# Kernel tuning notes

Measured on AMD Instinct MI355X. Metric: run time of the kernel, lower is better.

## Reference

```python
import jax, jax.numpy as jnp
import numpy as np

EPS = 1e-5

def _layer_norm(y, w, b):
    mu = y.mean(-1, keepdims=True)
    var = jnp.mean((y - mu) ** 2, axis=-1, keepdims=True)
    return (y - mu) * jax.lax.rsqrt(var + EPS) * w + b


def setup_inputs() -> dict:
    key = jax.random.key(0)
    ks = jax.random.split(key, 8)
    B, D, H, W = 1, 96, 96, 96
    N, R, K = 16, 6, 4
    x = jax.random.normal(ks[0], (B, D, H, W), jnp.float32)
    x_proj_weight = jax.random.normal(ks[1], (K, R + 2 * N, D), jnp.float32) * 0.05
    dt_projs_weight = jax.random.normal(ks[2], (K, D, R), jnp.float32) * 0.1
    dt_projs_bias = jax.random.normal(ks[3], (K, D), jnp.float32) * 0.1
    A_logs = jax.random.normal(ks[4], (K * D, N), jnp.float32)
    Ds = jax.random.normal(ks[5], (K * D,), jnp.float32) * 0.1
    ln_w = jnp.ones((D,), jnp.float32)
    ln_b = jnp.zeros((D,), jnp.float32)
    return {"x": x, "x_proj_weight": x_proj_weight, "dt_projs_weight": dt_projs_weight,
            "dt_projs_bias": dt_projs_bias, "A_logs": A_logs, "Ds": Ds,
            "ln_w": ln_w, "ln_b": ln_b}


def reference(x, x_proj_weight, dt_projs_weight, dt_projs_bias, A_logs, Ds, ln_w, ln_b):
    B, D, H, W = x.shape
    L = H * W
    K = x_proj_weight.shape[0]            # 4 scan directions
    N = A_logs.shape[1]                   # d_state
    R = dt_projs_weight.shape[2]          # dt_rank

    # ---- CrossScan: 4 directional flattenings -> xs [B, K, D, L]
    xs0 = x.reshape(B, D, L)
    xs1 = jnp.swapaxes(x, 2, 3).reshape(B, D, L)
    xs = jnp.stack([xs0, xs1, xs0[:, :, ::-1], xs1[:, :, ::-1]], axis=1)

    # ---- input-dependent projections
    x_dbl = jnp.einsum('bkdl,kcd->bkcl', xs, x_proj_weight)    # [B,K,R+2N,L]
    dts = x_dbl[:, :, :R]
    Bs = x_dbl[:, :, R:R + N]                                  # [B,K,N,L]
    Cs = x_dbl[:, :, R + N:]                                   # [B,K,N,L]
    dts = jnp.einsum('bkrl,kdr->bkdl', dts, dt_projs_weight)   # [B,K,D,L]

    # ---- selective scan (S6), delta_softplus=True, fp32
    delta = jax.nn.softplus(dts + dt_projs_bias[None, :, :, None])   # [B,K,D,L]
    A = -jnp.exp(A_logs).reshape(K, D, N)                             # [K,D,N]
    dA = jnp.exp(jnp.einsum('bkdl,kdn->bkdln', delta, A))             # [B,K,D,L,N]
    dBu = jnp.einsum('bkdl,bknl,bkdl->bkdln', delta, Bs, xs)          # delta*B*u

    def combine(c1, c2):
        a1, b1 = c1
        a2, b2 = c2
        return a1 * a2, a2 * b1 + b2

    _, h = jax.lax.associative_scan(combine, (dA, dBu), axis=3)       # h_t over L

    y = jnp.einsum('bkdln,bknl->bkdl', h, Cs)
    y = y + xs * Ds.reshape(K, D)[None, :, :, None]                   # [B,K,D,L]

    # ---- CrossMerge: undo the 4 directional scans and sum
    ys = y[:, 0:2] + y[:, 2:4, :, ::-1]                               # [B,2,D,L]
    ym = ys[:, 0] + jnp.swapaxes(ys[:, 1].reshape(B, D, W, H), 2, 3).reshape(B, D, L)

    # ---- out_norm (LayerNorm over D) and reshape to [B,H,W,D]
    yout = jnp.swapaxes(ym, 1, 2)                                     # [B,L,D]
    yout = _layer_norm(yout, ln_w, ln_b).reshape(B, H, W, D)
    return yout.astype(x.dtype)
```

## Files before the change

kernel.cpp:

```cpp
#include <hip/hip_runtime.h>
#include <math.h>

constexpr int cD = 96, cL = 9216, cK = 4;
constexpr int CL = 36, NCH = 256;
constexpr long cDL = (long)cD * cL;
constexpr float LOG2E = 1.44269504088896f;

constexpr long OFF_XT    = 0;
constexpr long OFF_DELTA = OFF_XT    + cDL;
constexpr long OFF_BC    = OFF_DELTA + 4L*cDL;
constexpr long OFF_Y     = OFF_BC    + 4L*cL*32;
constexpr long OFF_PG    = OFF_Y     + 4L*cDL;
constexpr long OFF_SG    = OFF_PG    + 384L*256*16;

__device__ __forceinline__ float4 a2prep(float4 v) {
    return make_float4(-LOG2E * exp2f(LOG2E * v.x), -LOG2E * exp2f(LOG2E * v.y),
                       -LOG2E * exp2f(LOG2E * v.z), -LOG2E * exp2f(LOG2E * v.w));
}
template<int C>
__device__ __forceinline__ float qperm(float v) {
    return __int_as_float(__builtin_amdgcn_mov_dpp(__float_as_int(v), C, 0xf, 0xf, true));
}

__global__ __launch_bounds__(256) void kT(const float* __restrict__ x,
                                          float* __restrict__ xT) {
    __shared__ float t[32][33];
    const int h0 = blockIdx.x * 32, w0 = blockIdx.y * 32, d = blockIdx.z;
    const float* xd = x + (long)d * cL;
    float* xtd = xT + (long)d * cL;
    for (int o = threadIdx.x; o < 1024; o += 256) {
        int i = o >> 5, j = o & 31;
        t[i][j] = xd[(h0 + i) * 96 + w0 + j];
    }
    __syncthreads();
    for (int o = threadIdx.x; o < 1024; o += 256) {
        int i = o >> 5, j = o & 31;
        xtd[(w0 + i) * 96 + h0 + j] = t[j][i];
    }
}

__global__ __launch_bounds__(256) void kA(const float* __restrict__ x,
                                          const float* __restrict__ xT,
                                          const float* __restrict__ xpw,
                                          const float* __restrict__ dtw,
                                          const float* __restrict__ dtb,
                                          float* __restrict__ delta,
                                          float* __restrict__ BC) {
    __shared__ float xs[96][64];
    __shared__ float xdbl[38][65];
    __shared__ float dtw_l[96 * 6];
    __shared__ float dtb_l[96];
    const int p0 = blockIdx.x * 64;
    const int k  = blockIdx.y;
    const int tid = threadIdx.x;
    const float* src = (k & 1) ? xT : x;

    for (int o = tid; o < 96 * 64; o += 256) {
        int dd = o >> 6, pp = o & 63;
        xs[dd][pp] = src[(long)dd * cL + p0 + pp];
    }
    for (int o = tid; o < 96 * 6; o += 256) dtw_l[o] = dtw[k * 96 * 6 + o];
    if (tid < 96) dtb_l[tid] = dtb[k * 96 + tid];
    __syncthreads();

    const int lane = tid & 63;
    const int c0 = __builtin_amdgcn_readfirstlane((tid >> 6) * 10);
    const float* wk = xpw + (long)k * 38 * 96;
    float acc[10];
    #pragma unroll
    for (int i = 0; i < 10; ++i) acc[i] = 0.f;
    #pragma unroll 4
    for (int dd = 0; dd < 96; ++dd) {
        float xv = xs[dd][lane];
        #pragma unroll
        for (int i = 0; i < 10; ++i) {
            int c = c0 + i; c = c > 37 ? 37 : c;
            acc[i] = fmaf(xv, wk[c * 96 + dd], acc[i]);
        }
    }
    #pragma unroll
    for (int i = 0; i < 10; ++i) {
        int c = c0 + i; c = c > 37 ? 37 : c;
        xdbl[c][lane] = acc[i];
    }
    __syncthreads();

    for (int o = tid; o < 64 * 16; o += 256) {
        int n = o & 15, pp = o >> 4;
        int P = p0 + pp;
        int q = (k < 2) ? P : (9215 - P);
        int ch = q / 36, j = q - ch * 36;
        long idx = (((long)k * 36 + j) * 256 + ch) * 32 + n;
        BC[idx]      = xdbl[6 + n][pp];
        BC[idx + 16] = xdbl[22 + n][pp];
    }
    for (int o = tid; o < 96 * 64; o += 256) {
        int dd = o >> 6, pp = o & 63;
        float s = dtb_l[dd];
        #pragma unroll
        for (int r = 0; r < 6; ++r) s = fmaf(xdbl[r][pp], dtw_l[dd * 6 + r], s);
        float sp = fmaxf(s, 0.f) + __logf(1.f + __expf(-fabsf(s)));
        delta[((long)(k * 96 + dd)) * cL + p0 + pp] = sp;
    }
}

__global__ __launch_bounds__(512, 6) void kS1(const float* __restrict__ x,
                                              const float* __restrict__ xT,
                                              const float* __restrict__ delta,
                                              const float* __restrict__ BC,
                                              const float* __restrict__ Alog,
                                              float* __restrict__ Pg,
                                              float* __restrict__ Sg) {
    __shared__ float dls[4608], xls[4608];
    const int tid = threadIdx.x;
    const int n0 = (tid & 3) * 4, chl = tid >> 2;
    const int hb = blockIdx.x & 1, seq = blockIdx.x >> 1;
    const int k = seq / 96, d = seq % 96, rev = k >> 1;
    const int ch = hb * 128 + chl;

    const float* dRow = delta + (long)seq * cL;
    const float* xRow = ((k & 1) ? xT : x) + (long)d * cL;
    const int sb2 = rev ? (1 - hb) * 4608 : hb * 4608;
    for (int o = tid; o < 1152; o += 512) {
        ((float4*)dls)[o] = ((const float4*)(dRow + sb2))[o];
        ((float4*)xls)[o] = ((const float4*)(xRow + sb2))[o];
    }
    const float4 a2 = a2prep(*(const float4*)(Alog + (long)seq * 16 + n0));
    const float* bc = BC + ((long)k * 36 * 256 + ch) * 32 + n0;
    __syncthreads();

    const int sbase = chl * 36;
    float4 h = make_float4(0.f, 0.f, 0.f, 0.f);
    float sdl = 0.f;
#define STEP1(DL, XV, B) { \
        float t = (DL) * (XV); sdl += (DL); \
        h.x = fmaf(exp2f((DL)*a2.x), h.x, t*(B).x); \
        h.y = fmaf(exp2f((DL)*a2.y), h.y, t*(B).y); \
        h.z = fmaf(exp2f((DL)*a2.z), h.z, t*(B).z); \
        h.w = fmaf(exp2f((DL)*a2.w), h.w, t*(B).w); }
    #pragma unroll
    for (int g = 0; g < 9; ++g) {
        const float* bj = bc + (long)(4 * g) * 8192;
        float4 B0 = *(const float4*)(bj);
        float4 B1 = *(const float4*)(bj + 8192);
        float4 B2 = *(const float4*)(bj + 16384);
        float4 B3 = *(const float4*)(bj + 24576);
        float4 d4, x4;
        if (!rev) {
            d4 = *(const float4*)(dls + sbase + 4 * g);
            x4 = *(const float4*)(xls + sbase + 4 * g);
            STEP1(d4.x, x4.x, B0) STEP1(d4.y, x4.y, B1)
            STEP1(d4.z, x4.z, B2) STEP1(d4.w, x4.w, B3)
        } else {
            d4 = *(const float4*)(dls + 4604 - sbase - 4 * g);
            x4 = *(const float4*)(xls + 4604 - sbase - 4 * g);
            STEP1(d4.w, x4.w, B0) STEP1(d4.z, x4.z, B1)
            STEP1(d4.y, x4.y, B2) STEP1(d4.x, x4.x, B3)
        }
    }
#undef STEP1
    long o = ((long)seq * NCH + ch) * 16 + n0;
    *(float4*)(Pg + o) = make_float4(exp2f(a2.x*sdl), exp2f(a2.y*sdl),
                                     exp2f(a2.z*sdl), exp2f(a2.w*sdl));
    *(float4*)(Sg + o) = h;
}

__global__ __launch_bounds__(256) void kC(float* __restrict__ Pg,
                                          const float* __restrict__ Sg) {
    __shared__ float gp[256], gs[256];
    const int seq = blockIdx.x;
    const int tid = threadIdx.x;
    const int sn = tid & 15, sg = tid >> 4;
    const long base = (long)seq * 4096 + sg * 256 + sn;

    float LPe[16], LSe[16];
    float P = 1.f, S = 0.f;
    #pragma unroll
    for (int i = 0; i < 16; ++i) {
        float p = Pg[base + i * 16], s = Sg[base + i * 16];
        LPe[i] = P; LSe[i] = S;
        S = fmaf(p, S, s); P *= p;
    }
    gp[tid] = P; gs[tid] = S;
    __syncthreads();
    #pragma unroll
    for (int off = 1; off < 16; off <<= 1) {
        float pc = gp[tid], sc = gs[tid];
        float pn = pc, s2 = sc;
        if (sg >= off) {
            pn = pc * gp[tid - off * 16];
            s2 = fmaf(pc, gs[tid - off * 16], sc);
        }
        __syncthreads();
        gp[tid] = pn; gs[tid] = s2;
        __syncthreads();
    }
    const float GS = (sg == 0) ? 0.f : gs[tid - 16];
    #pragma unroll
    for (int i = 0; i < 16; ++i)
        Pg[base + i * 16] = fmaf(LPe[i], GS, LSe[i]);
}

__global__ __launch_bounds__(256, 5) void kR(const float* __restrict__ x,
                                             const float* __restrict__ xT,
                                             const float* __restrict__ delta,
                                             const float* __restrict__ BC,
                                             const float* __restrict__ Alog,
                                             const float* __restrict__ Dsv,
                                             const float* __restrict__ hin,
                                             float* __restrict__ y) {
    __shared__ float dls[2304], xls[2304];
    __shared__ float ybuf[2304 + 24];
    const int tid = threadIdx.x;
    const int n0 = (tid & 3) * 4, chl = tid >> 2, r = tid & 3;
    const int qb = blockIdx.x & 3, seq = blockIdx.x >> 2;
    const int k = seq / 96, d = seq % 96, rev = k >> 1;
    const int ch = qb * 64 + chl;

    const float* dRow = delta + (long)seq * cL;
    const float* xRow = ((k & 1) ? xT : x) + (long)d * cL;
    const int sb = rev ? (3 - qb) * 2304 : qb * 2304;
    for (int o = tid; o < 576; o += 256) {
        ((float4*)dls)[o] = ((const float4*)(dRow + sb))[o];
        ((float4*)xls)[o] = ((const float4*)(xRow + sb))[o];
    }
    const float4 a2 = a2prep(*(const float4*)(Alog + (long)seq * 16 + n0));
    const float Dv = Dsv[seq];
    const float* bc = BC + ((long)k * 36 * 256 + ch) * 32 + n0;
    float4 h = *(const float4*)(hin + ((long)seq * NCH + ch) * 16 + n0);
    __syncthreads();

    const int sbase = chl * 36;
    float yhold = 0.f;
#define STEP2(DL, XV, B, C, SI) { \
        float t = (DL) * (XV); \
        h.x = fmaf(exp2f((DL)*a2.x), h.x, t*(B).x); \
        h.y = fmaf(exp2f((DL)*a2.y), h.y, t*(B).y); \
        h.z = fmaf(exp2f((DL)*a2.z), h.z, t*(B).z); \
        h.w = fmaf(exp2f((DL)*a2.w), h.w, t*(B).w); \
        float pv = fmaf(h.x, (C).x, fmaf(h.y, (C).y, fmaf(h.z, (C).z, h.w * (C).w))); \
        pv += qperm<0xB1>(pv); \
        pv += qperm<0x4E>(pv); \
        if ((SI) == r) yhold = fmaf(Dv, (XV), pv); }
    #pragma unroll
    for (int g = 0; g < 9; ++g) {
        const float* bj = bc + (long)(4 * g) * 8192;
        float4 B0 = *(const float4*)(bj);
        float4 C0 = *(const float4*)(bj + 16);
        float4 B1 = *(const float4*)(bj + 8192);
        float4 C1 = *(const float4*)(bj + 8192 + 16);
        float4 B2 = *(const float4*)(bj + 16384);
        float4 C2 = *(const float4*)(bj + 16384 + 16);
        float4 B3 = *(const float4*)(bj + 24576);
        float4 C3 = *(const float4*)(bj + 24576 + 16);
        float4 d4, x4;
        if (!rev) {
            d4 = *(const float4*)(dls + sbase + 4 * g);
            x4 = *(const float4*)(xls + sbase + 4 * g);
            STEP2(d4.x, x4.x, B0, C0, 0) STEP2(d4.y, x4.y, B1, C1, 1)
            STEP2(d4.z, x4.z, B2, C2, 2) STEP2(d4.w, x4.w, B3, C3, 3)
        } else {
            d4 = *(const float4*)(dls + 2300 - sbase - 4 * g);
            x4 = *(const float4*)(xls + 2300 - sbase - 4 * g);
            STEP2(d4.w, x4.w, B0, C0, 0) STEP2(d4.z, x4.z, B1, C1, 1)
            STEP2(d4.y, x4.y, B2, C2, 2) STEP2(d4.x, x4.x, B3, C3, 3)
        }
        int sl = sbase + 4 * g + r;
        int yloc = rev ? 2303 - sl : sl;
        ybuf[yloc + yloc / 96] = yhold;
    }
#undef STEP2
    __syncthreads();

    float* yrow = y + (long)seq * cL;
    if (k & 1) {
        const int w0 = sb / 96;
        for (int o = tid; o < 2304; o += 256) {
            int hh = o / 24, wl = o - hh * 24;
            yrow[hh * 96 + w0 + wl] = ybuf[wl * 97 + hh];
        }
    } else {
        for (int o = tid; o < 2304; o += 256) {
            yrow[sb + o] = ybuf[o + o / 96];
        }
    }
}

__global__ __launch_bounds__(256) void kE(const float* __restrict__ y,
                                          const float* __restrict__ lnw,
                                          const float* __restrict__ lnb,
                                          float* __restrict__ out) {
    __shared__ float vs[96][36];
    __shared__ float red[8][32], red2[8][32];
    __shared__ float MU[32], RS[32];
    const int tid = threadIdx.x;
    const int p0 = blockIdx.x * 32;

    for (int o = tid; o < 96 * 8; o += 256) {
        int dd = o >> 3, j = o & 7;
        const float* r0 = y + (long)dd * cL + p0;
        const float* r1 = y + cDL + (long)dd * cL + p0;
        const float* r2 = y + 2 * cDL + (long)dd * cL + p0;
        const float* r3 = y + 3 * cDL + (long)dd * cL + p0;
        float4 a = ((const float4*)r0)[j];
        float4 b = ((const float4*)r1)[j];
        float4 c = ((const float4*)r2)[j];
        float4 e = ((const float4*)r3)[j];
        *(float4*)&vs[dd][4 * j] = make_float4(a.x + b.x + c.x + e.x,
                                               a.y + b.y + c.y + e.y,
                                               a.z + b.z + c.z + e.z,
                                               a.w + b.w + c.w + e.w);
    }
    __syncthreads();

    const int p = tid & 31, part = tid >> 5;
    float s = 0.f, s2 = 0.f;
    for (int dd = part * 12; dd < part * 12 + 12; ++dd) {
        float v = vs[dd][p];
        s += v; s2 = fmaf(v, v, s2);
    }
    red[part][p] = s; red2[part][p] = s2;
    __syncthreads();
    if (tid < 32) {
        float S = 0.f, S2 = 0.f;
        #pragma unroll
        for (int q = 0; q < 8; ++q) { S += red[q][tid]; S2 += red2[q][tid]; }
        float m = S * (1.f / 96.f);
        MU[tid] = m;
        RS[tid] = rsqrtf(S2 * (1.f / 96.f) - m * m + 1e-5f);
    }
    __syncthreads();
    for (int o = tid; o < 32 * 96; o += 256) {
        int pl = o / 96, dd = o - pl * 96;
        out[(long)(p0 + pl) * 96 + dd] = (vs[dd][pl] - MU[pl]) * RS[pl] * lnw[dd] + lnb[dd];
    }
}

extern "C" void kernel_launch(void* const* d_in, const int* in_sizes, int n_in,
                              void* d_out, int out_size, void* d_ws, size_t ws_size,
                              hipStream_t stream) {
    const float* x    = (const float*)d_in[0];
    const float* xpw  = (const float*)d_in[1];
    const float* dtw  = (const float*)d_in[2];
    const float* dtb  = (const float*)d_in[3];
    const float* Alog = (const float*)d_in[4];
    const float* Dsv  = (const float*)d_in[5];
    const float* lnw  = (const float*)d_in[6];
    const float* lnb  = (const float*)d_in[7];
    float* ws = (float*)d_ws;

    float* xT    = ws + OFF_XT;
    float* delta = ws + OFF_DELTA;
    float* BC    = ws + OFF_BC;
    float* y     = ws + OFF_Y;
    float* Pg    = ws + OFF_PG;
    float* Sg    = ws + OFF_SG;
    float* out   = (float*)d_out;

    kT<<<dim3(3, 3, 96), 256, 0, stream>>>(x, xT);
    kA<<<dim3(144, 4), 256, 0, stream>>>(x, xT, xpw, dtw, dtb, delta, BC);
    kS1<<<768, 512, 0, stream>>>(x, xT, delta, BC, Alog, Pg, Sg);
    kC<<<384, 256, 0, stream>>>(Pg, Sg);
    kR<<<1536, 256, 0, stream>>>(x, xT, delta, BC, Alog, Dsv, Pg, y);
    kE<<<288, 256, 0, stream>>>(y, lnw, lnb, out);
}
```

Baseline: 92.09 us.

## Fuse chunked scan passes into one kernel with decoupled lookback across blocks

Merges the three scan kernels (chunk summary, carry combine, rescan) into a single kernel. Each block scans its quarter of a sequence, combines chunk carries in shared memory, publishes its aggregate with a flag, and then spins until the preceding quarters of the same sequence have published before doing the output pass. This removes two kernel launches and the global round-trip of per-chunk prefix state. In exchange it relies on earlier blocks being scheduled first, which risks deadlock or serialization, and it adds a memset plus spin-wait latency.

```diff
diff --git a/kernel.cpp b/kernel.cpp
--- a/kernel.cpp
+++ b/kernel.cpp
@@ -2,7 +2,7 @@
 #include <math.h>
 
 constexpr int cD = 96, cL = 9216, cK = 4;
-constexpr int CL = 36, NCH = 256;
+constexpr int CL = 36;
 constexpr long cDL = (long)cD * cL;
 constexpr float LOG2E = 1.44269504088896f;
 
@@ -10,8 +10,8 @@
 constexpr long OFF_DELTA = OFF_XT    + cDL;
 constexpr long OFF_BC    = OFF_DELTA + 4L*cDL;
 constexpr long OFF_Y     = OFF_BC    + 4L*cL*32;
-constexpr long OFF_PG    = OFF_Y     + 4L*cDL;
-constexpr long OFF_SG    = OFF_PG    + 384L*256*16;
+constexpr long OFF_QS    = OFF_Y     + 4L*cDL;
+constexpr long OFF_FLAGS = OFF_QS    + 384L*4*32;
 
 __device__ __forceinline__ float4 a2prep(float4 v) {
     return make_float4(-LOG2E * exp2f(LOG2E * v.x), -LOG2E * exp2f(LOG2E * v.y),
@@ -20,6 +20,12 @@
 template<int C>
 __device__ __forceinline__ float qperm(float v) {
     return __int_as_float(__builtin_amdgcn_mov_dpp(__float_as_int(v), C, 0xf, 0xf, true));
+}
+__device__ __forceinline__ void agent_store(float* p, float v) {
+    __hip_atomic_store(p, v, __ATOMIC_RELAXED, __HIP_MEMORY_SCOPE_AGENT);
+}
+__device__ __forceinline__ float agent_load(const float* p) {
+    return __hip_atomic_load(p, __ATOMIC_RELAXED, __HIP_MEMORY_SCOPE_AGENT);
 }
 
 __global__ __launch_bounds__(256) void kT(const float* __restrict__ x,
@@ -104,117 +110,24 @@
     }
 }
 
-__global__ __launch_bounds__(512, 6) void kS1(const float* __restrict__ x,
-                                              const float* __restrict__ xT,
-                                              const float* __restrict__ delta,
-                                              const float* __restrict__ BC,
-                                              const float* __restrict__ Alog,
-                                              float* __restrict__ Pg,
-                                              float* __restrict__ Sg) {
-    __shared__ float dls[4608], xls[4608];
+__global__ __launch_bounds__(256) void kS(const float* __restrict__ x,
+                                          const float* __restrict__ xT,
+                                          const float* __restrict__ delta,
+                                          const float* __restrict__ BC,
+                                          const float* __restrict__ Alog,
+                                          const float* __restrict__ Dsv,
+                                          float* __restrict__ Qs,
+                                          int* flags,
+                                          float* __restrict__ y) {
+    __shared__ float dls[2304], xls[2304];
+    __shared__ float lp[64][16], ls[64][16];
+    __shared__ float ybuf[2304 + 24];
+    float* gpf = &lp[0][0];
+    float* gsf = &ls[0][0];
     const int tid = threadIdx.x;
-    const int n0 = (tid & 3) * 4, chl = tid >> 2;
-    const int hb = blockIdx.x & 1, seq = blockIdx.x >> 1;
-    const int k = seq / 96, d = seq % 96, rev = k >> 1;
-    const int ch = hb * 128 + chl;
-
-    const float* dRow = delta + (long)seq * cL;
-    const float* xRow = ((k & 1) ? xT : x) + (long)d * cL;
-    const int sb2 = rev ? (1 - hb) * 4608 : hb * 4608;
-    for (int o = tid; o < 1152; o += 512) {
-        ((float4*)dls)[o] = ((const float4*)(dRow + sb2))[o];
-        ((float4*)xls)[o] = ((const float4*)(xRow + sb2))[o];
-    }
-    const float4 a2 = a2prep(*(const float4*)(Alog + (long)seq * 16 + n0));
-    const float* bc = BC + ((long)k * 36 * 256 + ch) * 32 + n0;
-    __syncthreads();
-
-    const int sbase = chl * 36;
-    float4 h = make_float4(0.f, 0.f, 0.f, 0.f);
-    float sdl = 0.f;
-#define STEP1(DL, XV, B) { \
-        float t = (DL) * (XV); sdl += (DL); \
-        h.x = fmaf(exp2f((DL)*a2.x), h.x, t*(B).x); \
-        h.y = fmaf(exp2f((DL)*a2.y), h.y, t*(B).y); \
-        h.z = fmaf(exp2f((DL)*a2.z), h.z, t*(B).z); \
-        h.w = fmaf(exp2f((DL)*a2.w), h.w, t*(B).w); }
-    #pragma unroll
-    for (int g = 0; g < 9; ++g) {
-        const float* bj = bc + (long)(4 * g) * 8192;
-        float4 B0 = *(const float4*)(bj);
-        float4 B1 = *(const float4*)(bj + 8192);
-        float4 B2 = *(const float4*)(bj + 16384);
-        float4 B3 = *(const float4*)(bj + 24576);
-        float4 d4, x4;
-        if (!rev) {
-            d4 = *(const float4*)(dls + sbase + 4 * g);
-            x4 = *(const float4*)(xls + sbase + 4 * g);
-            STEP1(d4.x, x4.x, B0) STEP1(d4.y, x4.y, B1)
-            STEP1(d4.z, x4.z, B2) STEP1(d4.w, x4.w, B3)
-        } else {
-            d4 = *(const float4*)(dls + 4604 - sbase - 4 * g);
-            x4 = *(const float4*)(xls + 4604 - sbase - 4 * g);
-            STEP1(d4.w, x4.w, B0) STEP1(d4.z, x4.z, B1)
-            STEP1(d4.y, x4.y, B2) STEP1(d4.x, x4.x, B3)
-        }
-    }
-#undef STEP1
-    long o = ((long)seq * NCH + ch) * 16 + n0;
-    *(float4*)(Pg + o) = make_float4(exp2f(a2.x*sdl), exp2f(a2.y*sdl),
-                                     exp2f(a2.z*sdl), exp2f(a2.w*sdl));
-    *(float4*)(Sg + o) = h;
-}
-
-__global__ __launch_bounds__(256) void kC(float* __restrict__ Pg,
-                                          const float* __restrict__ Sg) {
-    __shared__ float gp[256], gs[256];
-    const int seq = blockIdx.x;
-    const int tid = threadIdx.x;
-    const int sn = tid & 15, sg = tid >> 4;
-    const long base = (long)seq * 4096 + sg * 256 + sn;
-
-    float LPe[16], LSe[16];
-    float P = 1.f, S = 0.f;
-    #pragma unroll
-    for (int i = 0; i < 16; ++i) {
-        float p = Pg[base + i * 16], s = Sg[base + i * 16];
-        LPe[i] = P; LSe[i] = S;
-        S = fmaf(p, S, s); P *= p;
-    }
-    gp[tid] = P; gs[tid] = S;
-    __syncthreads();
-    #pragma unroll
-    for (int off = 1; off < 16; off <<= 1) {
-        float pc = gp[tid], sc = gs[tid];
-        float pn = pc, s2 = sc;
-        if (sg >= off) {
-            pn = pc * gp[tid - off * 16];
-            s2 = fmaf(pc, gs[tid - off * 16], sc);
-        }
-        __syncthreads();
-        gp[tid] = pn; gs[tid] = s2;
-        __syncthreads();
-    }
-    const float GS = (sg == 0) ? 0.f : gs[tid - 16];
-    #pragma unroll
-    for (int i = 0; i < 16; ++i)
-        Pg[base + i * 16] = fmaf(LPe[i], GS, LSe[i]);
-}
-
-__global__ __launch_bounds__(256, 5) void kR(const float* __restrict__ x,
-                                             const float* __restrict__ xT,
-                                             const float* __restrict__ delta,
-                                             const float* __restrict__ BC,
-                                             const float* __restrict__ Alog,
-                                             const float* __restrict__ Dsv,
-                                             const float* __restrict__ hin,
-                                             float* __restrict__ y) {
-    __shared__ float dls[2304], xls[2304];
-    __shared__ float ybuf[2304 + 24];
-    const int tid = threadIdx.x;
-    const int n0 = (tid & 3) * 4, chl = tid >> 2, r = tid & 3;
     const int qb = blockIdx.x & 3, seq = blockIdx.x >> 2;
     const int k = seq / 96, d = seq % 96, rev = k >> 1;
+    const int n0 = (tid & 3) * 4, chl = tid >> 2, r = tid & 3;
     const int ch = qb * 64 + chl;
 
     const float* dRow = delta + (long)seq * cL;
@@ -225,14 +138,128 @@
         ((float4*)xls)[o] = ((const float4*)(xRow + sb))[o];
     }
     const float4 a2 = a2prep(*(const float4*)(Alog + (long)seq * 16 + n0));
+    const float* bc = BC + ((long)k * 36 * 256 + ch) * 32 + n0;
+    __syncthreads();
+
+    const int sbase = chl * 36;
+    {
+        float4 h = make_float4(0.f, 0.f, 0.f, 0.f);
+        float sdl = 0.f;
+#define ST1(DL, XV, B) { \
+        float t = (DL) * (XV); sdl += (DL); \
+        h.x = fmaf(exp2f((DL)*a2.x), h.x, t*(B).x); \
+        h.y = fmaf(exp2f((DL)*a2.y), h.y, t*(B).y); \
+        h.z = fmaf(exp2f((DL)*a2.z), h.z, t*(B).z); \
+        h.w = fmaf(exp2f((DL)*a2.w), h.w, t*(B).w); }
+        #pragma unroll
+        for (int g = 0; g < 9; ++g) {
+            const float* bj = bc + (long)(4 * g) * 8192;
+            float4 B0 = *(const float4*)(bj);
+            float4 B1 = *(const float4*)(bj + 8192);
+            float4 B2 = *(const float4*)(bj + 16384);
+            float4 B3 = *(const float4*)(bj + 24576);
+            float4 d4, x4;
+            if (!rev) {
+                d4 = *(const float4*)(dls + sbase + 4 * g);
+                x4 = *(const float4*)(xls + sbase + 4 * g);
+                ST1(d4.x, x4.x, B0) ST1(d4.y, x4.y, B1)
+                ST1(d4.z, x4.z, B2) ST1(d4.w, x4.w, B3)
+            } else {
+                d4 = *(const float4*)(dls + 2300 - sbase - 4 * g);
+                x4 = *(const float4*)(xls + 2300 - sbase - 4 * g);
+                ST1(d4.w, x4.w, B0) ST1(d4.z, x4.z, B1)
+                ST1(d4.y, x4.y, B2) ST1(d4.x, x4.x, B3)
+            }
+        }
+#undef ST1
+        *(float4*)&lp[chl][n0] = make_float4(exp2f(a2.x*sdl), exp2f(a2.y*sdl),
+                                             exp2f(a2.z*sdl), exp2f(a2.w*sdl));
+        *(float4*)&ls[chl][n0] = h;
+    }
+    __syncthreads();
+
+    const int sn = tid & 15, sg = tid >> 4;
+    float LPe[4], LSe[4];
+    {
+        float P = 1.f, S = 0.f;
+        #pragma unroll
+        for (int i = 0; i < 4; ++i) {
+            LPe[i] = P; LSe[i] = S;
+            float p = lp[sg * 4 + i][sn], s = ls[sg * 4 + i][sn];
+            S = fmaf(p, S, s); P *= p;
+        }
+        __syncthreads();
+        gpf[tid] = P; gsf[tid] = S;
+    }
+    __syncthreads();
+    #pragma unroll
+    for (int off = 1; off < 16; off <<= 1) {
+        float pc = gpf[tid], sc = gsf[tid];
+        float pn = pc, snn = sc;
+        if (sg >= off) {
+            pn  = pc * gpf[tid - off * 16];
+            snn = fmaf(pc, gsf[tid - off * 16], sc);
+        }
+        __syncthreads();
+        gpf[tid] = pn; gsf[tid] = snn;
+        __syncthreads();
+    }
+    const float GPx = (sg == 0) ? 1.f : gpf[tid - 16];
+    const float GSx = (sg == 0) ? 0.f : gsf[tid - 16];
+    if (tid < 16) {
+        float* q = Qs + ((long)seq * 4 + qb) * 32;
+        agent_store(q + tid,      gpf[240 + tid]);
+        agent_store(q + 16 + tid, gsf[240 + tid]);
+    }
+    float Pex[4], Sex[4];
+    #pragma unroll
+    for (int i = 0; i < 4; ++i) {
+        Pex[i] = GPx * LPe[i];
+        Sex[i] = fmaf(LPe[i], GSx, LSe[i]);
+    }
+    __syncthreads();
+
+    if (tid == 0) {
+        __hip_atomic_store(&flags[(seq << 2) + qb], 1, __ATOMIC_RELEASE,
+                           __HIP_MEMORY_SCOPE_AGENT);
+    }
+
+    #pragma unroll
+    for (int i = 0; i < 4; ++i) {
+        lp[sg * 4 + i][sn] = Pex[i];
+        ls[sg * 4 + i][sn] = Sex[i];
+    }
+    __syncthreads();
+
+    float4 hq = make_float4(0.f, 0.f, 0.f, 0.f);
+    if (qb > 0) {
+        if (tid < qb) {
+            while (__hip_atomic_load(&flags[(seq << 2) + tid], __ATOMIC_ACQUIRE,
+                                     __HIP_MEMORY_SCOPE_AGENT) == 0) {
+                __builtin_amdgcn_s_sleep(1);
+            }
+        }
+        __syncthreads();
+        for (int j = 0; j < qb; ++j) {
+            const float* q = Qs + ((long)seq * 4 + j) * 32 + n0;
+            float4 Pj = make_float4(agent_load(q + 0), agent_load(q + 1),
+                                    agent_load(q + 2), agent_load(q + 3));
+            float4 Sj = make_float4(agent_load(q + 16), agent_load(q + 17),
+                                    agent_load(q + 18), agent_load(q + 19));
+            hq.x = fmaf(Pj.x, hq.x, Sj.x);
+            hq.y = fmaf(Pj.y, hq.y, Sj.y);
+            hq.z = fmaf(Pj.z, hq.z, Sj.z);
+            hq.w = fmaf(Pj.w, hq.w, Sj.w);
+        }
+    }
+    float4 lpv = *(float4*)&lp[chl][n0];
+    float4 lsv = *(float4*)&ls[chl][n0];
+    float4 h = make_float4(fmaf(lpv.x, hq.x, lsv.x), fmaf(lpv.y, hq.y, lsv.y),
+                           fmaf(lpv.z, hq.z, lsv.z), fmaf(lpv.w, hq.w, lsv.w));
+
     const float Dv = Dsv[seq];
-    const float* bc = BC + ((long)k * 36 * 256 + ch) * 32 + n0;
-    float4 h = *(const float4*)(hin + ((long)seq * NCH + ch) * 16 + n0);
-    __syncthreads();
-
-    const int sbase = chl * 36;
     float yhold = 0.f;
-#define STEP2(DL, XV, B, C, SI) { \
+#define ST2(DL, XV, B, C, SI) { \
         float t = (DL) * (XV); \
         h.x = fmaf(exp2f((DL)*a2.x), h.x, t*(B).x); \
         h.y = fmaf(exp2f((DL)*a2.y), h.y, t*(B).y); \
@@ -257,19 +284,19 @@
         if (!rev) {
             d4 = *(const float4*)(dls + sbase + 4 * g);
             x4 = *(const float4*)(xls + sbase + 4 * g);
-            STEP2(d4.x, x4.x, B0, C0, 0) STEP2(d4.y, x4.y, B1, C1, 1)
-            STEP2(d4.z, x4.z, B2, C2, 2) STEP2(d4.w, x4.w, B3, C3, 3)
+            ST2(d4.x, x4.x, B0, C0, 0) ST2(d4.y, x4.y, B1, C1, 1)
+            ST2(d4.z, x4.z, B2, C2, 2) ST2(d4.w, x4.w, B3, C3, 3)
         } else {
             d4 = *(const float4*)(dls + 2300 - sbase - 4 * g);
             x4 = *(const float4*)(xls + 2300 - sbase - 4 * g);
-            STEP2(d4.w, x4.w, B0, C0, 0) STEP2(d4.z, x4.z, B1, C1, 1)
-            STEP2(d4.y, x4.y, B2, C2, 2) STEP2(d4.x, x4.x, B3, C3, 3)
+            ST2(d4.w, x4.w, B0, C0, 0) ST2(d4.z, x4.z, B1, C1, 1)
+            ST2(d4.y, x4.y, B2, C2, 2) ST2(d4.x, x4.x, B3, C3, 3)
         }
         int sl = sbase + 4 * g + r;
         int yloc = rev ? 2303 - sl : sl;
         ybuf[yloc + yloc / 96] = yhold;
     }
-#undef STEP2
+#undef ST2
     __syncthreads();
 
     float* yrow = y + (long)seq * cL;
@@ -353,14 +380,13 @@
     float* delta = ws + OFF_DELTA;
     float* BC    = ws + OFF_BC;
     float* y     = ws + OFF_Y;
-    float* Pg    = ws + OFF_PG;
-    float* Sg    = ws + OFF_SG;
+    float* Qs    = ws + OFF_QS;
+    int*   flags = (int*)(ws + OFF_FLAGS);
     float* out   = (float*)d_out;
 
+    hipMemsetAsync(flags, 0, 1536 * sizeof(int), stream);
     kT<<<dim3(3, 3, 96), 256, 0, stream>>>(x, xT);
     kA<<<dim3(144, 4), 256, 0, stream>>>(x, xT, xpw, dtw, dtb, delta, BC);
-    kS1<<<768, 512, 0, stream>>>(x, xT, delta, BC, Alog, Pg, Sg);
-    kC<<<384, 256, 0, stream>>>(Pg, Sg);
-    kR<<<1536, 256, 0, stream>>>(x, xT, delta, BC, Alog, Dsv, Pg, y);
+    kS<<<1536, 256, 0, stream>>>(x, xT, delta, BC, Alog, Dsv, Qs, flags, y);
     kE<<<288, 256, 0, stream>>>(y, lnw, lnb, out);
 }
```

Measured after the change: 127.4 us. 1.38x slower.
